# Optimization experiments

Hardware: AMD Instinct MI355X
Metric: run time of the kernel (lower is better)

The kernel has to match this reference:

```python
import jax, jax.numpy as jnp
import numpy as np

BLOCK = 32          # per_1x32 microscaling block size along K
FP4_MAX = 6.0       # largest magnitude representable in e2m1
FP4_EMAX = 2.0      # exponent of largest fp4 binade (4..6)


def _quant_dequant_mxfp4(x):
    """Simulate MXFP4 (e2m1 elements, shared power-of-two E8M0 scale per 1x32
    block along the last dim): quantize then dequantize. x: [..., K], K % 32 == 0."""
    shape = x.shape
    xb = x.reshape(*shape[:-1], shape[-1] // BLOCK, BLOCK)
    amax = jnp.max(jnp.abs(xb), axis=-1, keepdims=True)
    # shared scale: 2^(floor(log2(amax)) - emax) so the block max lands in the top binade
    exp = jnp.floor(jnp.log2(jnp.maximum(amax, jnp.finfo(x.dtype).tiny))) - FP4_EMAX
    scale = jnp.where(amax > 0, jnp.exp2(exp), jnp.ones_like(amax))
    q = jnp.clip(xb / scale, -FP4_MAX, FP4_MAX)
    aq = jnp.abs(q)
    # e2m1 ulp: 0.5 on [0,2), 1 on [2,4), 2 on [4,6]
    lsb = jnp.where(aq < 2.0, 0.5, jnp.where(aq < 4.0, 1.0, 2.0))
    qr = jnp.round(q / lsb) * lsb  # round-to-nearest-even onto the fp4 grid
    return (qr * scale).reshape(shape)


def setup_inputs() -> dict:
    key = jax.random.key(0)
    k1, k2, k3 = jax.random.split(key, 3)
    B, S, K, N = 4, 2048, 2048, 2048
    inp = jax.random.normal(k1, (B, S, K), dtype=jnp.float32)
    weight = jax.random.normal(k2, (N, K), dtype=jnp.float32) * (1.0 / np.sqrt(K))
    bias = jax.random.normal(k3, (N,), dtype=jnp.float32) * 0.02
    return {"input": inp, "weight": weight, "bias": bias}


def reference(input, weight, bias):
    # both activation and weight are fake-quantized to MXFP4 per 1x32 blocks
    # along the contraction (in_features) dim, then a standard GEMM + bias.
    orig_shape = input.shape
    a = _quant_dequant_mxfp4(input.reshape(-1, orig_shape[-1]))  # [M, K]
    w = _quant_dequant_mxfp4(weight)                              # [N, K]
    out = jnp.einsum("mk,nk->mn", a, w) + bias
    return out.reshape(*orig_shape[:-1], weight.shape[0])
```

## Files before the change

### kernel.cpp

```cpp
#include <hip/hip_runtime.h>
#include <cstdint>


#define BM 256
#define BN 256
#define BK 128
#define NBUF 4

typedef float floatx4 __attribute__((ext_vector_type(4)));
typedef int intx8 __attribute__((ext_vector_type(8)));

#define GLOBAL_AS __attribute__((address_space(1)))
#define LDS_AS __attribute__((address_space(3)))


__device__ __forceinline__ int enc1(float x, float inv) {
    float q = x * inv;
    q = fminf(fmaxf(q, -6.0f), 6.0f);
    int s = (int)(__float_as_uint(q) >> 31) << 3;
    float aq = fabsf(q);
    float ilsb = aq < 2.0f ? 2.0f : (aq < 4.0f ? 1.0f : 0.5f);
    float lsb  = aq < 2.0f ? 0.5f : (aq < 4.0f ? 1.0f : 2.0f);
    float ar = rintf(aq * ilsb) * lsb;
    int c;
    if (ar < 2.0f)      c = (int)(ar * 2.0f);
    else if (ar < 4.0f) c = 2 + (int)ar;
    else                c = 4 + (int)(ar * 0.5f);
    return c | s;
}

__global__ void quant_mxfp4_v3(const float* __restrict__ A, uint8_t* __restrict__ Aq,
                               uint8_t* __restrict__ Asc,
                               const float* __restrict__ W, uint8_t* __restrict__ Wq,
                               uint8_t* __restrict__ Wsc,
                               long na4, long ntot4) {
    long t = (long)blockIdx.x * 256 + threadIdx.x;
    if (t >= ntot4) return;
    const float* src; uint8_t* dq; uint8_t* ds; long idx;
    if (t < na4) { src = A; dq = Aq; ds = Asc; idx = t; }
    else         { src = W; dq = Wq; ds = Wsc; idx = t - na4; }

    float4 f = ((const float4*)src)[idx];
    float amax = fmaxf(fmaxf(fabsf(f.x), fabsf(f.y)),
                       fmaxf(fabsf(f.z), fabsf(f.w)));
    amax = fmaxf(amax, __shfl_xor(amax, 1));
    amax = fmaxf(amax, __shfl_xor(amax, 2));
    amax = fmaxf(amax, __shfl_xor(amax, 4));

    int ebits = (int)((__float_as_uint(amax) >> 23) & 0xff);
    int sb;
    float inv;
    if (amax > 0.0f) {
        sb = ebits - 2; if (sb < 0) sb = 0;
        inv = __uint_as_float((unsigned)((256 - ebits) & 255) << 23);
    } else {
        sb = 127;
        inv = 0.0f;
    }

    int c0 = enc1(f.x, inv), c1 = enc1(f.y, inv);
    int c2 = enc1(f.z, inv), c3 = enc1(f.w, inv);
    ((unsigned short*)dq)[idx] =
        (unsigned short)(c0 | (c1 << 4) | (c2 << 8) | (c3 << 12));
    if ((idx & 7) == 0) ds[idx >> 3] = (uint8_t)sb;
}


__global__ __launch_bounds__(512, 2) void gemm_fp4_pipe(
        const uint8_t* __restrict__ Aq, const uint8_t* __restrict__ Asc,
        const uint8_t* __restrict__ Wq, const uint8_t* __restrict__ Wsc,
        const float* __restrict__ bias, float* __restrict__ C,
        int M, int N, int K) {
    __shared__ __align__(16) uint8_t sA[NBUF][BM * BK / 2];
    __shared__ __align__(16) uint8_t sB[NBUF][BN * BK / 2];
    __shared__ __align__(16) uint8_t sSA[NBUF][BM * 4];
    __shared__ __align__(16) uint8_t sSB[NBUF][BN * 4];

    const int tid = threadIdx.x;
    const int lane = tid & 63;
    const int w = tid >> 6;
    const int wr = w >> 2;
    const int wc = w & 3;
    const int row16 = lane & 15;
    const int quad = lane >> 4;
    const int shq = quad * 8;
    const int m0 = blockIdx.y * BM;
    const int n0 = blockIdx.x * BN;
    const int KB2 = K >> 1, KB32 = K >> 5;
    const int NT = K / BK;

    const int fragoff = (quad ^ ((row16 ^ (row16 >> 2)) & 3)) * 16;
    const int aRow = wr * 128 + row16;
    const int bRow = wc * 64 + row16;

    floatx4 acc[8][4];
#pragma unroll
    for (int i = 0; i < 8; i++)
#pragma unroll
        for (int j = 0; j < 4; j++) acc[i][j] = (floatx4){0.f, 0.f, 0.f, 0.f};

    auto stageA = [&](int tt) {
        const int bb = tt & (NBUF - 1);
        const int kb = tt * (BK / 2);
#pragma unroll
        for (int it = 0; it < 2; ++it) {
            int idx = it * 512 + tid;
            int row = idx >> 2, c = idx & 3;
            int g = c ^ ((row ^ (row >> 2)) & 3);
            const uint8_t* src = Aq + (size_t)(m0 + row) * KB2 + kb + g * 16;
            __builtin_amdgcn_global_load_lds((GLOBAL_AS void*)src,
                (LDS_AS void*)(&sA[bb][idx * 16]), 16, 0, 0);
        }
        int r2 = tid & 255;
        if (tid < 256) {
            const uint8_t* src = Asc + (size_t)(m0 + r2) * KB32 + tt * 4;
            __builtin_amdgcn_global_load_lds((GLOBAL_AS void*)src,
                (LDS_AS void*)(&sSA[bb][r2 * 4]), 4, 0, 0);
        } else {
            const uint8_t* src = Wsc + (size_t)(n0 + r2) * KB32 + tt * 4;
            __builtin_amdgcn_global_load_lds((GLOBAL_AS void*)src,
                (LDS_AS void*)(&sSB[bb][r2 * 4]), 4, 0, 0);
        }
    };
    auto stageB = [&](int tt) {
        const int bb = tt & (NBUF - 1);
        const int kb = tt * (BK / 2);
#pragma unroll
        for (int it = 0; it < 2; ++it) {
            int idx = it * 512 + tid;
            int row = idx >> 2, c = idx & 3;
            int g = c ^ ((row ^ (row >> 2)) & 3);
            const uint8_t* src = Wq + (size_t)(n0 + row) * KB2 + kb + g * 16;
            __builtin_amdgcn_global_load_lds((GLOBAL_AS void*)src,
                (LDS_AS void*)(&sB[bb][idx * 16]), 16, 0, 0);
        }
    };
    auto fence = [] {
        __builtin_amdgcn_sched_barrier(0);
        __builtin_amdgcn_s_barrier();
    };

    stageA(0); stageB(0);
    if (NT > 1) { stageA(1); stageB(1); }
    if (NT > 2) { stageA(2); stageB(2); }
    if (NT > 2)      asm volatile("s_waitcnt vmcnt(10)" ::: "memory");
    else if (NT > 1) asm volatile("s_waitcnt vmcnt(5)" ::: "memory");
    else             asm volatile("s_waitcnt vmcnt(0)" ::: "memory");
    fence();

    for (int t = 0; t < NT; ++t) {
        const int p = t & (NBUF - 1);
        const uint8_t* pa = sA[p];
        const uint8_t* pb = sB[p];

        int4 bfr[4], afr[4];
        int sw32[4], sa32[4];
#pragma unroll
        for (int ni = 0; ni < 4; ++ni) {
            int r = bRow + ni * 16;
            bfr[ni] = *(const int4*)(pb + r * 64 + fragoff);
            sw32[ni] = *(const int*)(&sSB[p][r * 4]);
        }
#pragma unroll
        for (int mi = 0; mi < 4; ++mi) {
            int r = aRow + mi * 16;
            afr[mi] = *(const int4*)(pa + r * 64 + fragoff);
            sa32[mi] = *(const int*)(&sSA[p][r * 4]);
        }
        if (t + 3 < NT) stageA(t + 3);
        fence();

        int swb[4], sab[4];
#pragma unroll
        for (int ni = 0; ni < 4; ++ni) swb[ni] = (sw32[ni] >> shq) & 0xff;
#pragma unroll
        for (int mi = 0; mi < 4; ++mi) sab[mi] = (sa32[mi] >> shq) & 0xff;

        __builtin_amdgcn_s_setprio(1);
#pragma unroll
        for (int mi = 0; mi < 4; ++mi) {
            intx8 a8 = {afr[mi].x, afr[mi].y, afr[mi].z, afr[mi].w, 0, 0, 0, 0};
#pragma unroll
            for (int ni = 0; ni < 4; ++ni) {
                intx8 b8 = {bfr[ni].x, bfr[ni].y, bfr[ni].z, bfr[ni].w, 0, 0, 0, 0};
                acc[mi][ni] = __builtin_amdgcn_mfma_scale_f32_16x16x128_f8f6f4(
                    a8, b8, acc[mi][ni], 4, 4, 0, sab[mi], 0, swb[ni]);
            }
        }
        __builtin_amdgcn_s_setprio(0);
        fence();

#pragma unroll
        for (int mi = 0; mi < 4; ++mi) {
            int r = aRow + (mi + 4) * 16;
            afr[mi] = *(const int4*)(pa + r * 64 + fragoff);
            sa32[mi] = *(const int*)(&sSA[p][r * 4]);
        }
        if (t + 3 < NT) stageB(t + 3);
        fence();

#pragma unroll
        for (int mi = 0; mi < 4; ++mi) sab[mi] = (sa32[mi] >> shq) & 0xff;

        __builtin_amdgcn_s_setprio(1);
#pragma unroll
        for (int mi = 0; mi < 4; ++mi) {
            intx8 a8 = {afr[mi].x, afr[mi].y, afr[mi].z, afr[mi].w, 0, 0, 0, 0};
#pragma unroll
            for (int ni = 0; ni < 4; ++ni) {
                intx8 b8 = {bfr[ni].x, bfr[ni].y, bfr[ni].z, bfr[ni].w, 0, 0, 0, 0};
                acc[mi + 4][ni] = __builtin_amdgcn_mfma_scale_f32_16x16x128_f8f6f4(
                    a8, b8, acc[mi + 4][ni], 4, 4, 0, sab[mi], 0, swb[ni]);
            }
        }
        __builtin_amdgcn_s_setprio(0);

        if (t < NT - 1) {
            int rem = NT - 2 - t;
            if (rem >= 2)      asm volatile("s_waitcnt vmcnt(10)" ::: "memory");
            else if (rem == 1) asm volatile("s_waitcnt vmcnt(5)" ::: "memory");
            else               asm volatile("s_waitcnt vmcnt(0)" ::: "memory");
        }
        fence();
    }

#pragma unroll
    for (int ni = 0; ni < 4; ++ni) {
        int n = n0 + wc * 64 + ni * 16 + row16;
        float bv = bias[n];
#pragma unroll
        for (int mi = 0; mi < 8; ++mi) {
            int mbase = m0 + wr * 128 + mi * 16 + quad * 4;
#pragma unroll
            for (int r = 0; r < 4; ++r) {
                C[(size_t)(mbase + r) * N + n] = acc[mi][ni][r] + bv;
            }
        }
    }
}


extern "C" void kernel_launch(void* const* d_in, const int* in_sizes, int n_in,
                              void* d_out, int out_size, void* d_ws, size_t ws_size,
                              hipStream_t stream) {
    const float* inp  = (const float*)d_in[0];
    const float* wgt  = (const float*)d_in[1];
    const float* bias = (const float*)d_in[2];
    float* out = (float*)d_out;

    const int N = in_sizes[2];
    const int K = in_sizes[1] / N;
    const long M = (long)in_sizes[0] / K;

    uint8_t* Aq4 = (uint8_t*)d_ws;
    uint8_t* Wq4 = Aq4 + (size_t)M * K / 2;
    uint8_t* Asc = Wq4 + (size_t)N * K / 2;
    uint8_t* Wsc = Asc + (size_t)M * K / 32;

    long na4   = (long)M * K / 4;
    long ntot4 = na4 + (long)N * K / 4;
    quant_mxfp4_v3<<<dim3((ntot4 + 255) / 256), dim3(256), 0, stream>>>(
        inp, Aq4, Asc, wgt, Wq4, Wsc, na4, ntot4);

    dim3 grid(N / BN, (int)(M / BM));
    gemm_fp4_pipe<<<grid, dim3(512), 0, stream>>>(
        Aq4, Asc, Wq4, Wsc, bias, out, (int)M, N, K);
}
```

Baseline: 159.4 us.

## Shrink GEMM tiles to 128x128 with double buffering and swizzled block order

```diff
diff --git a/kernel.cpp b/kernel.cpp
--- a/kernel.cpp
+++ b/kernel.cpp
@@ -2,10 +2,10 @@
 #include <cstdint>
 
 
-#define BM 256
-#define BN 256
+#define BM 128
+#define BN 128
 #define BK 128
-#define NBUF 4
+#define NBUF 2
 
 typedef float floatx4 __attribute__((ext_vector_type(4)));
 typedef int intx8 __attribute__((ext_vector_type(8)));
@@ -66,7 +66,7 @@
 }
 
 
-__global__ __launch_bounds__(512, 2) void gemm_fp4_pipe(
+__global__ __launch_bounds__(256, 3) void gemm_fp4_pipe(
         const uint8_t* __restrict__ Aq, const uint8_t* __restrict__ Asc,
         const uint8_t* __restrict__ Wq, const uint8_t* __restrict__ Wsc,
         const float* __restrict__ bias, float* __restrict__ C,
@@ -79,149 +79,118 @@
     const int tid = threadIdx.x;
     const int lane = tid & 63;
     const int w = tid >> 6;
-    const int wr = w >> 2;
-    const int wc = w & 3;
+    const int wr = w >> 1;
+    const int wc = w & 1;
     const int row16 = lane & 15;
     const int quad = lane >> 4;
     const int shq = quad * 8;
-    const int m0 = blockIdx.y * BM;
-    const int n0 = blockIdx.x * BN;
+
+    const int id = blockIdx.x;
+    const int g = id & 7, h = id >> 3;
+    const int by = g + 8 * (h & 7);
+    const int bx = h >> 3;
+    const int m0 = by * BM;
+    const int n0 = bx * BN;
     const int KB2 = K >> 1, KB32 = K >> 5;
     const int NT = K / BK;
 
     const int fragoff = (quad ^ ((row16 ^ (row16 >> 2)) & 3)) * 16;
-    const int aRow = wr * 128 + row16;
-    const int bRow = wc * 64 + row16;
-
-    floatx4 acc[8][4];
-#pragma unroll
-    for (int i = 0; i < 8; i++)
+    const int rA = wr * 64 + row16;
+    const int rB = wc * 64 + row16;
+
+    floatx4 acc[4][4];
+#pragma unroll
+    for (int i = 0; i < 4; i++)
 #pragma unroll
         for (int j = 0; j < 4; j++) acc[i][j] = (floatx4){0.f, 0.f, 0.f, 0.f};
 
-    auto stageA = [&](int tt) {
-        const int bb = tt & (NBUF - 1);
+    auto stage = [&](int tt) {
+        const int bb = tt & 1;
         const int kb = tt * (BK / 2);
 #pragma unroll
         for (int it = 0; it < 2; ++it) {
-            int idx = it * 512 + tid;
+            int idx = it * 256 + tid;
             int row = idx >> 2, c = idx & 3;
-            int g = c ^ ((row ^ (row >> 2)) & 3);
-            const uint8_t* src = Aq + (size_t)(m0 + row) * KB2 + kb + g * 16;
+            int gsw = c ^ ((row ^ (row >> 2)) & 3);
+            const uint8_t* src = Aq + (size_t)(m0 + row) * KB2 + kb + gsw * 16;
             __builtin_amdgcn_global_load_lds((GLOBAL_AS void*)src,
                 (LDS_AS void*)(&sA[bb][idx * 16]), 16, 0, 0);
         }
-        int r2 = tid & 255;
-        if (tid < 256) {
-            const uint8_t* src = Asc + (size_t)(m0 + r2) * KB32 + tt * 4;
-            __builtin_amdgcn_global_load_lds((GLOBAL_AS void*)src,
-                (LDS_AS void*)(&sSA[bb][r2 * 4]), 4, 0, 0);
+#pragma unroll
+        for (int it = 0; it < 2; ++it) {
+            int idx = it * 256 + tid;
+            int row = idx >> 2, c = idx & 3;
+            int gsw = c ^ ((row ^ (row >> 2)) & 3);
+            const uint8_t* src = Wq + (size_t)(n0 + row) * KB2 + kb + gsw * 16;
+            __builtin_amdgcn_global_load_lds((GLOBAL_AS void*)src,
+                (LDS_AS void*)(&sB[bb][idx * 16]), 16, 0, 0);
+        }
+        if (tid < 128) {
+            const uint8_t* src = Asc + (size_t)(m0 + tid) * KB32 + tt * 4;
+            __builtin_amdgcn_global_load_lds((GLOBAL_AS void*)src,
+                (LDS_AS void*)(&sSA[bb][tid * 4]), 4, 0, 0);
         } else {
-            const uint8_t* src = Wsc + (size_t)(n0 + r2) * KB32 + tt * 4;
-            __builtin_amdgcn_global_load_lds((GLOBAL_AS void*)src,
-                (LDS_AS void*)(&sSB[bb][r2 * 4]), 4, 0, 0);
+            const uint8_t* src = Wsc + (size_t)(n0 + tid - 128) * KB32 + tt * 4;
+            __builtin_amdgcn_global_load_lds((GLOBAL_AS void*)src,
+                (LDS_AS void*)(&sSB[bb][(tid - 128) * 4]), 4, 0, 0);
         }
     };
-    auto stageB = [&](int tt) {
-        const int bb = tt & (NBUF - 1);
-        const int kb = tt * (BK / 2);
-#pragma unroll
-        for (int it = 0; it < 2; ++it) {
-            int idx = it * 512 + tid;
-            int row = idx >> 2, c = idx & 3;
-            int g = c ^ ((row ^ (row >> 2)) & 3);
-            const uint8_t* src = Wq + (size_t)(n0 + row) * KB2 + kb + g * 16;
-            __builtin_amdgcn_global_load_lds((GLOBAL_AS void*)src,
-                (LDS_AS void*)(&sB[bb][idx * 16]), 16, 0, 0);
-        }
-    };
-    auto fence = [] {
+
+    stage(0);
+    if (NT > 1) stage(1);
+    if (NT > 1) asm volatile("s_waitcnt vmcnt(5)" ::: "memory");
+    else        asm volatile("s_waitcnt vmcnt(0)" ::: "memory");
+    __builtin_amdgcn_sched_barrier(0);
+    __builtin_amdgcn_s_barrier();
+    __builtin_amdgcn_sched_barrier(0);
+
+    for (int t = 0; t < NT; ++t) {
+        const int p = t & 1;
+        const uint8_t* pa = sA[p];
+        const uint8_t* pb = sB[p];
+
+        intx8 A8[4], B8[4];
+        int sab[4], swb[4];
+#pragma unroll
+        for (int ni = 0; ni < 4; ++ni) {
+            int r = rB + ni * 16;
+            int4 f = *(const int4*)(pb + r * 64 + fragoff);
+            B8[ni] = (intx8){f.x, f.y, f.z, f.w, 0, 0, 0, 0};
+            swb[ni] = (*(const int*)(&sSB[p][r * 4]) >> shq) & 0xff;
+        }
+#pragma unroll
+        for (int mi = 0; mi < 4; ++mi) {
+            int r = rA + mi * 16;
+            int4 f = *(const int4*)(pa + r * 64 + fragoff);
+            A8[mi] = (intx8){f.x, f.y, f.z, f.w, 0, 0, 0, 0};
+            sab[mi] = (*(const int*)(&sSA[p][r * 4]) >> shq) & 0xff;
+        }
+
+        asm volatile("s_waitcnt lgkmcnt(0)" ::: "memory");
         __builtin_amdgcn_sched_barrier(0);
         __builtin_amdgcn_s_barrier();
-    };
-
-    stageA(0); stageB(0);
-    if (NT > 1) { stageA(1); stageB(1); }
-    if (NT > 2) { stageA(2); stageB(2); }
-    if (NT > 2)      asm volatile("s_waitcnt vmcnt(10)" ::: "memory");
-    else if (NT > 1) asm volatile("s_waitcnt vmcnt(5)" ::: "memory");
-    else             asm volatile("s_waitcnt vmcnt(0)" ::: "memory");
-    fence();
-
-    for (int t = 0; t < NT; ++t) {
-        const int p = t & (NBUF - 1);
-        const uint8_t* pa = sA[p];
-        const uint8_t* pb = sB[p];
-
-        int4 bfr[4], afr[4];
-        int sw32[4], sa32[4];
-#pragma unroll
-        for (int ni = 0; ni < 4; ++ni) {
-            int r = bRow + ni * 16;
-            bfr[ni] = *(const int4*)(pb + r * 64 + fragoff);
-            sw32[ni] = *(const int*)(&sSB[p][r * 4]);
-        }
+        __builtin_amdgcn_sched_barrier(0);
+
+        if (t + 2 < NT) stage(t + 2);
+
+        __builtin_amdgcn_s_setprio(1);
 #pragma unroll
         for (int mi = 0; mi < 4; ++mi) {
-            int r = aRow + mi * 16;
-            afr[mi] = *(const int4*)(pa + r * 64 + fragoff);
-            sa32[mi] = *(const int*)(&sSA[p][r * 4]);
-        }
-        if (t + 3 < NT) stageA(t + 3);
-        fence();
-
-        int swb[4], sab[4];
-#pragma unroll
-        for (int ni = 0; ni < 4; ++ni) swb[ni] = (sw32[ni] >> shq) & 0xff;
-#pragma unroll
-        for (int mi = 0; mi < 4; ++mi) sab[mi] = (sa32[mi] >> shq) & 0xff;
-
-        __builtin_amdgcn_s_setprio(1);
-#pragma unroll
-        for (int mi = 0; mi < 4; ++mi) {
-            intx8 a8 = {afr[mi].x, afr[mi].y, afr[mi].z, afr[mi].w, 0, 0, 0, 0};
 #pragma unroll
             for (int ni = 0; ni < 4; ++ni) {
-                intx8 b8 = {bfr[ni].x, bfr[ni].y, bfr[ni].z, bfr[ni].w, 0, 0, 0, 0};
                 acc[mi][ni] = __builtin_amdgcn_mfma_scale_f32_16x16x128_f8f6f4(
-                    a8, b8, acc[mi][ni], 4, 4, 0, sab[mi], 0, swb[ni]);
+                    A8[mi], B8[ni], acc[mi][ni], 4, 4, 0, sab[mi], 0, swb[ni]);
             }
         }
         __builtin_amdgcn_s_setprio(0);
-        fence();
-
-#pragma unroll
-        for (int mi = 0; mi < 4; ++mi) {
-            int r = aRow + (mi + 4) * 16;
-            afr[mi] = *(const int4*)(pa + r * 64 + fragoff);
-            sa32[mi] = *(const int*)(&sSA[p][r * 4]);
-        }
-        if (t + 3 < NT) stageB(t + 3);
-        fence();
-
-#pragma unroll
-        for (int mi = 0; mi < 4; ++mi) sab[mi] = (sa32[mi] >> shq) & 0xff;
-
-        __builtin_amdgcn_s_setprio(1);
-#pragma unroll
-        for (int mi = 0; mi < 4; ++mi) {
-            intx8 a8 = {afr[mi].x, afr[mi].y, afr[mi].z, afr[mi].w, 0, 0, 0, 0};
-#pragma unroll
-            for (int ni = 0; ni < 4; ++ni) {
-                intx8 b8 = {bfr[ni].x, bfr[ni].y, bfr[ni].z, bfr[ni].w, 0, 0, 0, 0};
-                acc[mi + 4][ni] = __builtin_amdgcn_mfma_scale_f32_16x16x128_f8f6f4(
-                    a8, b8, acc[mi + 4][ni], 4, 4, 0, sab[mi], 0, swb[ni]);
-            }
-        }
-        __builtin_amdgcn_s_setprio(0);
 
         if (t < NT - 1) {
-            int rem = NT - 2 - t;
-            if (rem >= 2)      asm volatile("s_waitcnt vmcnt(10)" ::: "memory");
-            else if (rem == 1) asm volatile("s_waitcnt vmcnt(5)" ::: "memory");
-            else               asm volatile("s_waitcnt vmcnt(0)" ::: "memory");
-        }
-        fence();
+            if (t + 2 < NT) asm volatile("s_waitcnt vmcnt(5)" ::: "memory");
+            else            asm volatile("s_waitcnt vmcnt(0)" ::: "memory");
+            __builtin_amdgcn_sched_barrier(0);
+            __builtin_amdgcn_s_barrier();
+            __builtin_amdgcn_sched_barrier(0);
+        }
     }
 
 #pragma unroll
@@ -229,8 +198,8 @@
         int n = n0 + wc * 64 + ni * 16 + row16;
         float bv = bias[n];
 #pragma unroll
-        for (int mi = 0; mi < 8; ++mi) {
-            int mbase = m0 + wr * 128 + mi * 16 + quad * 4;
+        for (int mi = 0; mi < 4; ++mi) {
+            int mbase = m0 + wr * 64 + mi * 16 + quad * 4;
 #pragma unroll
             for (int r = 0; r < 4; ++r) {
                 C[(size_t)(mbase + r) * N + n] = acc[mi][ni][r] + bv;
@@ -262,7 +231,7 @@
     quant_mxfp4_v3<<<dim3((ntot4 + 255) / 256), dim3(256), 0, stream>>>(
         inp, Aq4, Asc, wgt, Wq4, Wsc, na4, ntot4);
 
-    dim3 grid(N / BN, (int)(M / BM));
-    gemm_fp4_pipe<<<grid, dim3(512), 0, stream>>>(
+    dim3 grid((N / BN) * (int)(M / BM));
+    gemm_fp4_pipe<<<grid, dim3(256), 0, stream>>>(
         Aq4, Asc, Wq4, Wsc, bias, out, (int)M, N, K);
 }
```

New measurement: 160.2 us. No clear change (+0.5%).
